# Kernel tuning notes

Hardware: AMD Instinct MI355X
Metric: run time of the kernel (lower is better)

## Reference

```python
import jax, jax.numpy as jnp
import numpy as np
import math

LS = [0, 1, 2]            # degrees present in all irreps
MAX_L = 2
MULT_IN = 64
MULT_MID = 16
MULT_OUT = 64
N = 20000

# ---- Clebsch-Gordan coefficients in the real spherical-harmonic basis ----

def _f(n):
    return math.factorial(int(n))

def _cg_complex(j1, m1, j2, m2, j3, m3):
    if m1 + m2 != m3:
        return 0.0
    pre = math.sqrt((2 * j3 + 1) * _f(j1 + j2 - j3) * _f(j1 - j2 + j3) * _f(-j1 + j2 + j3) / _f(j1 + j2 + j3 + 1))
    pre *= math.sqrt(_f(j1 + m1) * _f(j1 - m1) * _f(j2 + m2) * _f(j2 - m2) * _f(j3 + m3) * _f(j3 - m3))
    kmin = max(0, j2 - j3 - m1, j1 - j3 + m2)
    kmax = min(j1 + j2 - j3, j1 - m1, j2 + m2)
    s = 0.0
    for k in range(kmin, kmax + 1):
        s += (-1) ** k / (_f(k) * _f(j1 + j2 - j3 - k) * _f(j1 - m1 - k) * _f(j2 + m2 - k) * _f(j3 - j2 + m1 + k) * _f(j3 - j1 - m2 + k))
    return pre * s

def _q(l):
    # complex->real change of basis, rows indexed by real m = -l..l
    Q = np.zeros((2 * l + 1, 2 * l + 1), dtype=complex)
    Q[l, l] = 1.0
    r2 = math.sqrt(2.0)
    for m in range(1, l + 1):
        Q[l + m, l + m] = (-1) ** m / r2
        Q[l + m, l - m] = 1.0 / r2
        Q[l - m, l - m] = 1j / r2
        Q[l - m, l + m] = -1j * (-1) ** m / r2
    return Q

def _real_cg(l1, l2, l3):
    C = np.zeros((2 * l1 + 1, 2 * l2 + 1, 2 * l3 + 1), dtype=complex)
    for m1 in range(-l1, l1 + 1):
        for m2 in range(-l2, l2 + 1):
            m3 = m1 + m2
            if -l3 <= m3 <= l3:
                C[l1 + m1, l2 + m2, l3 + m3] = _cg_complex(l1, m1, l2, m2, l3, m3)
    Q1, Q2, Q3 = _q(l1), _q(l2), _q(l3)
    M = np.einsum('ia,jb,kc,abc->ijk', Q1.conj(), Q2.conj(), Q3, C)
    if np.abs(M.imag).max() > np.abs(M.real).max():
        M = M * (-1j)  # fix parity phase so coefficients are real
    assert np.abs(M.imag).max() < 1e-10
    return np.asarray(M.real, dtype=np.float32)

# triangle-rule paths, truncated at MAX_L
PATHS = [(l1, l2, l) for l1 in LS for l2 in LS for l in range(abs(l1 - l2), min(l1 + l2, MAX_L) + 1)]
CG = {p: jnp.asarray(_real_cg(*p)) for p in PATHS}


def setup_inputs() -> dict:
    key = jax.random.key(0)
    ks = jax.random.split(key, 12)
    inp = {}
    for i, l in enumerate(LS):
        inp[f'x{l}'] = jax.random.normal(ks[i], (N, MULT_IN, 2 * l + 1), dtype=jnp.float32)
    for i, l in enumerate(LS):
        inp[f'W1_{l}'] = jax.random.normal(ks[3 + i], (MULT_IN, MULT_MID), dtype=jnp.float32)
        inp[f'W2_{l}'] = jax.random.normal(ks[6 + i], (MULT_IN, MULT_MID), dtype=jnp.float32)
    tp_mults = {l: sum(MULT_MID * MULT_MID for (l1, l2, lo) in PATHS if lo == l) for l in LS}
    for i, l in enumerate(LS):
        inp[f'W3_{l}'] = jax.random.normal(ks[9 + i], (tp_mults[l], MULT_OUT), dtype=jnp.float32)
    return inp


def _linear(x, W):
    # x: [n, u, i], W: [u, v] -> [n, v, i], normalized like e3nn Linear
    return jnp.einsum('nui,uv->nvi', x, W) / np.float32(math.sqrt(x.shape[1]))


def reference(x0, x1, x2, W1_0, W1_1, W1_2, W2_0, W2_1, W2_2, W3_0, W3_1, W3_2):
    xs = [x0, x1, x2]
    W1 = [W1_0, W1_1, W1_2]
    W2 = [W2_0, W2_1, W2_2]
    W3 = [W3_0, W3_1, W3_2]
    a = [_linear(xs[l], W1[l]) for l in LS]   # branch 1
    b = [_linear(xs[l], W2[l]) for l in LS]   # branch 2
    # CG tensor product up to MAX_L, full (uv) multiplicity
    tp = {l: [] for l in LS}
    n = x0.shape[0]
    for (l1, l2, l) in PATHS:
        t = jnp.einsum('nui,nvj,ijk->nuvk', a[l1], b[l2], CG[(l1, l2, l)])
        tp[l].append(t.reshape(n, MULT_MID * MULT_MID, 2 * l + 1))
    outs = []
    for l in LS:
        z = jnp.concatenate(tp[l], axis=1)        # [n, tp_mult_l, 2l+1]
        y = _linear(z, W3[l])                     # [n, MULT_OUT, 2l+1]
        outs.append(y.reshape(n, -1))
    return jnp.concatenate(outs, axis=1)          # [n, MULT_OUT * 9]
```

## Files before the change

### kernel.cpp

```cpp
#include <hip/hip_runtime.h>


typedef __attribute__((ext_vector_type(4))) float f32x4;
typedef __attribute__((ext_vector_type(8))) short short8;
typedef unsigned short ushort_t;
typedef unsigned int uint32;

__device__ __forceinline__ uint32 bfb(float x) {
  uint32 u = __float_as_uint(x);
  return (u + 0x7fffu + ((u >> 16) & 1u)) >> 16;
}
__device__ __forceinline__ uint32 pack2(float lo, float hi) {
  return bfb(lo) | (bfb(hi) << 16);
}

#define C2   0.7071067811865476f
#define C3   0.5773502691896258f
#define C5   0.4472135954999579f
#define C6   0.4082482904638631f
#define C23  0.8164965809277260f
#define C10  0.3162277660168379f
#define C210 0.6324555320336759f
#define C310 0.5477225575051661f
#define C14  0.2672612419124244f
#define C214 0.5345224838248488f
#define C314 0.4629100498862757f

__global__ __launch_bounds__(256) void pack_w3_kernel(
    const float* __restrict__ W30, const float* __restrict__ W31,
    const float* __restrict__ W32, ushort_t* __restrict__ pack) {
  int lc = blockIdx.x;
  int t = threadIdx.x >> 6;
  int lam = threadIdx.x & 63;
  const float* W;
  int mb;
  float nrm;
  if (lc < 24) {
    W = W30; mb = lc * 32; nrm = 0.036084391824351615f;
  } else if (lc < 72) {
    W = W31; mb = (lc - 24) * 32; nrm = 0.025515518153991442f;
  } else {
    W = W32; mb = (lc - 72) * 32; nrm = 0.025515518153991442f;
  }
  int w = t * 16 + (lam & 15);
  int m0 = mb + (lam >> 4) * 8;
  ushort_t* dst = pack + ((size_t)(lc * 4 + t) * 64 + lam) * 8;
#pragma unroll
  for (int j = 0; j < 8; ++j)
    dst[j] = (ushort_t)bfb(W[(size_t)(m0 + j) * 64 + w] * nrm);
}

template <int NK, class F>
__device__ __forceinline__ void zgen_path(const float* bsrow, int boff, int s, int u,
                                          ushort_t* zs, F f) {
  uint32 zp[NK][8];
#pragma unroll
  for (int v2 = 0; v2 < 8; ++v2) {
    float z0[NK], z1[NK];
    f(bsrow + (2 * v2) * 12 + boff, z0);
    f(bsrow + (2 * v2 + 1) * 12 + boff, z1);
#pragma unroll
    for (int k = 0; k < NK; ++k) zp[k][v2] = pack2(z0[k], z1[k]);
  }
#pragma unroll
  for (int k = 0; k < NK; ++k) {
    uint32* dst = (uint32*)(zs + (k * 16 + s) * 264 + u * 16);
    *(uint4*)(dst) = make_uint4(zp[k][0], zp[k][1], zp[k][2], zp[k][3]);
    *(uint4*)(dst + 4) = make_uint4(zp[k][4], zp[k][5], zp[k][6], zp[k][7]);
  }
}

template <int NROW>
__device__ __forceinline__ void mfma_acc(const ushort_t* zs, const ushort_t* pack,
                                         int pcbase, int wt, int lane, f32x4* acc) {
  int srow = lane & 15, quad = lane >> 4;
  const ushort_t* ab = zs + srow * 264 + quad * 8;
  const ushort_t* bb = pack + ((size_t)(pcbase * 4 + wt) * 64 + lane) * 8;
#pragma unroll
  for (int c = 0; c < 8; ++c) {
    short8 B = *(const short8*)(bb + (size_t)c * 2048);
#pragma unroll
    for (int rt = 0; rt < NROW; ++rt) {
      short8 A = *(const short8*)(ab + rt * 16 * 264 + c * 32);
      acc[rt] = __builtin_amdgcn_mfma_f32_16x16x32_bf16(A, B, acc[rt], 0, 0, 0);
    }
  }
}

__global__ __launch_bounds__(256) void tdense_kernel(
    const float* __restrict__ x0, const float* __restrict__ x1,
    const float* __restrict__ x2, const float* __restrict__ W10,
    const float* __restrict__ W20, const float* __restrict__ W11,
    const float* __restrict__ W21, const float* __restrict__ W12,
    const float* __restrict__ W22, const ushort_t* __restrict__ pack,
    float* __restrict__ out) {
  __shared__ float a_s[2304];
  __shared__ float b_s[3072];
  __shared__ __align__(16) ushort_t z_s[21120];

  const int tid = threadIdx.x;
  const int nbase = blockIdx.x * 16;

  for (int it = tid; it < 512; it += 256) {
    int brn = it >> 8;
    int s = (it >> 4) & 15;
    int v = it & 15;
    int n = nbase + s;
    const float* Wl0 = brn ? W20 : W10;
    const float* Wl1 = brn ? W21 : W11;
    const float* Wl2 = brn ? W22 : W12;
    const float* px0 = x0 + (size_t)n * 64;
    const float* px1 = x1 + (size_t)n * 192;
    const float* px2 = x2 + (size_t)n * 320;
    float s0 = 0.f, s1a = 0.f, s1b = 0.f, s1c = 0.f;
    float s2[5] = {0.f, 0.f, 0.f, 0.f, 0.f};
    for (int u = 0; u < 64; ++u) {
      float w0 = Wl0[u * 16 + v];
      float w1 = Wl1[u * 16 + v];
      float w2 = Wl2[u * 16 + v];
      s0 += px0[u] * w0;
      s1a += px1[u * 3 + 0] * w1;
      s1b += px1[u * 3 + 1] * w1;
      s1c += px1[u * 3 + 2] * w1;
#pragma unroll
      for (int j = 0; j < 5; ++j) s2[j] += px2[u * 5 + j] * w2;
    }
    float* dst = brn ? (b_s + (s * 16 + v) * 12) : (a_s + (s * 16 + v) * 9);
    dst[0] = s0 * 0.125f;
    dst[1] = s1a * 0.125f;
    dst[2] = s1b * 0.125f;
    dst[3] = s1c * 0.125f;
#pragma unroll
    for (int j = 0; j < 5; ++j) dst[4 + j] = s2[j] * 0.125f;
  }

  const int lane = tid & 63, wt = tid >> 6;
  const int zs_s = tid >> 4, zu = tid & 15;

  f32x4 acc0[1], acc1[3], acc2[5];
#pragma unroll
  for (int i = 0; i < 1; ++i) acc0[i] = (f32x4)(0.f);
#pragma unroll
  for (int i = 0; i < 3; ++i) acc1[i] = (f32x4)(0.f);
#pragma unroll
  for (int i = 0; i < 5; ++i) acc2[i] = (f32x4)(0.f);

  __syncthreads();

  float ar[9];
  {
    const float* arow = a_s + (zs_s * 16 + zu) * 9;
#pragma unroll
    for (int i = 0; i < 9; ++i) ar[i] = arow[i];
  }
  const float* bsrow = b_s + zs_s * 16 * 12;

#define RUN_PATH(NK, BOFF, PC, ACC, BODY)                         \
  zgen_path<NK>(bsrow, BOFF, zs_s, zu, z_s,                       \
                [&](const float* b, float* z) BODY);              \
  __syncthreads();                                                \
  mfma_acc<NK>(z_s, pack, PC, wt, lane, ACC);                     \
  __syncthreads();

  RUN_PATH(1, 0, 0, acc0, { z[0] = ar[0] * b[0]; })
  RUN_PATH(3, 1, 24, acc1, {
    z[0] = ar[0] * b[0]; z[1] = ar[0] * b[1]; z[2] = ar[0] * b[2];
  })
  RUN_PATH(5, 4, 72, acc2, {
    z[0] = ar[0] * b[0]; z[1] = ar[0] * b[1]; z[2] = ar[0] * b[2];
    z[3] = ar[0] * b[3]; z[4] = ar[0] * b[4];
  })
  RUN_PATH(3, 0, 32, acc1, {
    z[0] = ar[1] * b[0]; z[1] = ar[2] * b[0]; z[2] = ar[3] * b[0];
  })
  RUN_PATH(1, 1, 8, acc0, {
    z[0] = -C3 * (ar[1] * b[0] + ar[2] * b[1] + ar[3] * b[2]);
  })
  RUN_PATH(3, 1, 40, acc1, {
    z[0] = C2 * (ar[2] * b[2] - ar[3] * b[1]);
    z[1] = C2 * (ar[3] * b[0] - ar[1] * b[2]);
    z[2] = C2 * (ar[1] * b[1] - ar[2] * b[0]);
  })
  RUN_PATH(5, 1, 80, acc2, {
    z[0] = C2 * (ar[1] * b[2] + ar[3] * b[0]);
    z[1] = C2 * (ar[2] * b[0] + ar[1] * b[1]);
    z[2] = C23 * ar[2] * b[1] - C6 * (ar[1] * b[0] + ar[3] * b[2]);
    z[3] = C2 * (ar[2] * b[2] + ar[3] * b[1]);
    z[4] = C2 * (ar[3] * b[2] - ar[1] * b[0]);
  })
  RUN_PATH(3, 4, 48, acc1, {
    z[0] = -C310 * ar[2] * b[1] + C10 * ar[1] * b[2] - C310 * ar[3] * b[0] + C310 * ar[1] * b[4];
    z[1] = -C210 * ar[2] * b[2] - C310 * ar[3] * b[3] - C310 * ar[1] * b[1];
    z[2] = -C310 * ar[2] * b[3] + C10 * ar[3] * b[2] - C310 * ar[1] * b[0] - C310 * ar[3] * b[4];
  })
  RUN_PATH(5, 4, 88, acc2, {
    z[0] = C23 * ar[2] * b[4] + C6 * ar[1] * b[1] - C6 * ar[3] * b[3];
    z[1] = C6 * ar[2] * b[3] - C6 * ar[1] * b[0] - C2 * ar[3] * b[2] - C6 * ar[3] * b[4];
    z[2] = C2 * (ar[3] * b[1] - ar[1] * b[3]);
    z[3] = -C6 * ar[2] * b[1] + C2 * ar[1] * b[2] + C6 * ar[3] * b[0] - C6 * ar[1] * b[4];
    z[4] = -C23 * ar[2] * b[0] + C6 * ar[1] * b[3] + C6 * ar[3] * b[1];
  })
  RUN_PATH(5, 0, 96, acc2, {
    z[0] = ar[4] * b[0]; z[1] = ar[5] * b[0]; z[2] = ar[6] * b[0];
    z[3] = ar[7] * b[0]; z[4] = ar[8] * b[0];
  })
  RUN_PATH(3, 1, 56, acc1, {
    z[0] = -C310 * ar[5] * b[1] + C10 * ar[6] * b[0] - C310 * ar[4] * b[2] + C310 * ar[8] * b[0];
    z[1] = -C210 * ar[6] * b[1] - C310 * ar[7] * b[2] - C310 * ar[5] * b[0];
    z[2] = -C310 * ar[7] * b[1] + C10 * ar[6] * b[2] - C310 * ar[4] * b[0] - C310 * ar[8] * b[2];
  })
  RUN_PATH(5, 1, 104, acc2, {
    z[0] = -C23 * ar[8] * b[1] - C6 * ar[5] * b[0] + C6 * ar[7] * b[2];
    z[1] = -C6 * ar[7] * b[1] + C6 * ar[4] * b[0] + C2 * ar[6] * b[2] + C6 * ar[8] * b[2];
    z[2] = C2 * (ar[7] * b[0] - ar[5] * b[2]);
    z[3] = C6 * ar[5] * b[1] - C2 * ar[6] * b[0] - C6 * ar[4] * b[2] + C6 * ar[8] * b[0];
    z[4] = C23 * ar[4] * b[1] - C6 * ar[7] * b[0] - C6 * ar[5] * b[2];
  })
  RUN_PATH(1, 4, 16, acc0, {
    z[0] = C5 * (ar[4] * b[0] + ar[5] * b[1] + ar[6] * b[2] + ar[7] * b[3] + ar[8] * b[4]);
  })
  RUN_PATH(3, 4, 64, acc1, {
    z[0] = C10 * (ar[8] * b[3] - ar[7] * b[4] + ar[4] * b[1] - ar[5] * b[0]) +
           C310 * (ar[7] * b[2] - ar[6] * b[3]);
    z[1] = C10 * (ar[5] * b[3] - ar[7] * b[1]) + C210 * (ar[4] * b[4] - ar[8] * b[0]);
    z[2] = C10 * (ar[8] * b[1] - ar[5] * b[4] + ar[7] * b[0] - ar[4] * b[3]) +
           C310 * (ar[6] * b[1] - ar[5] * b[2]);
  })
  RUN_PATH(5, 4, 112, acc2, {
    z[0] = C214 * (ar[6] * b[0] + ar[4] * b[2]) - C314 * (ar[5] * b[3] + ar[7] * b[1]);
    z[1] = -C14 * (ar[6] * b[1] + ar[5] * b[2]) + C314 * (ar[5] * b[4] + ar[8] * b[1]) -
           C314 * (ar[7] * b[0] + ar[4] * b[3]);
    z[2] = -C214 * ar[6] * b[2] - C14 * (ar[5] * b[1] + ar[7] * b[3]) +
           C214 * (ar[4] * b[0] + ar[8] * b[4]);
    z[3] = -C14 * (ar[6] * b[3] + ar[7] * b[2]) - C314 * (ar[5] * b[0] + ar[4] * b[1]) -
           C314 * (ar[7] * b[4] + ar[8] * b[3]);
    z[4] = C214 * (ar[6] * b[4] + ar[8] * b[2]) + C314 * (ar[5] * b[1] - ar[7] * b[3]);
  })
#undef RUN_PATH

  {
    const int col = lane & 15, quad = lane >> 4;
    const int w = wt * 16 + col;
#pragma unroll
    for (int r = 0; r < 4; ++r) {
      int s = quad * 4 + r;
      float* row = out + (size_t)(nbase + s) * 576;
      row[w] = acc0[0][r];
      row[64 + w * 3 + 0] = acc1[0][r];
      row[64 + w * 3 + 1] = acc1[1][r];
      row[64 + w * 3 + 2] = acc1[2][r];
#pragma unroll
      for (int k = 0; k < 5; ++k) row[256 + w * 5 + k] = acc2[k][r];
    }
  }
}

extern "C" void kernel_launch(void* const* d_in, const int* in_sizes, int n_in,
                              void* d_out, int out_size, void* d_ws, size_t ws_size,
                              hipStream_t stream) {
  const float* x0 = (const float*)d_in[0];
  const float* x1 = (const float*)d_in[1];
  const float* x2 = (const float*)d_in[2];
  const float* W10 = (const float*)d_in[3];
  const float* W20 = (const float*)d_in[4];
  const float* W11 = (const float*)d_in[5];
  const float* W21 = (const float*)d_in[6];
  const float* W12 = (const float*)d_in[7];
  const float* W22 = (const float*)d_in[8];
  const float* W30 = (const float*)d_in[9];
  const float* W31 = (const float*)d_in[10];
  const float* W32 = (const float*)d_in[11];
  ushort_t* pack = (ushort_t*)d_ws;

  hipLaunchKernelGGL(pack_w3_kernel, dim3(120), dim3(256), 0, stream,
                     W30, W31, W32, pack);

  int nsamp = in_sizes[0] / 64;
  int nblocks = nsamp / 16;
  hipLaunchKernelGGL(tdense_kernel, dim3(nblocks), dim3(256), 0, stream,
                     x0, x1, x2, W10, W20, W11, W21, W12, W22, pack,
                     (float*)d_out);
}
```

Before: 259.5 us.

## Batch CG paths per barrier, vectorize projections, cheaper bf16 packing

The first-stage projections now run in one pass per thread, computing both branches with vectorized float4 loads of x. The a-projection stays in registers, and b is stored transposed to shared memory so the z-generation can load it as vectors. Several CG paths are grouped into one shared-memory z buffer per synchronization phase, which cuts the number of barriers. The bf16 conversion switches to a cheaper round-half-up pack using a byte permute, which slightly changes the rounding behavior. The z buffer grows and launch_bounds now requests 2 blocks per CU, which may constrain registers.

Result: faster. 222.7 us (-14.2%).

```diff
diff --git a/kernel.cpp b/kernel.cpp
--- a/kernel.cpp
+++ b/kernel.cpp
@@ -2,6 +2,8 @@
 
 
 typedef __attribute__((ext_vector_type(4))) float f32x4;
+typedef __attribute__((ext_vector_type(4))) float f4;
+typedef __attribute__((ext_vector_type(2))) float f2;
 typedef __attribute__((ext_vector_type(8))) short short8;
 typedef unsigned short ushort_t;
 typedef unsigned int uint32;
@@ -10,8 +12,11 @@
   uint32 u = __float_as_uint(x);
   return (u + 0x7fffu + ((u >> 16) & 1u)) >> 16;
 }
-__device__ __forceinline__ uint32 pack2(float lo, float hi) {
-  return bfb(lo) | (bfb(hi) << 16);
+
+__device__ __forceinline__ uint32 pack2f(f2 z) {
+  uint32 lo = __float_as_uint(z.x) + 0x8000u;
+  uint32 hi = __float_as_uint(z.y) + 0x8000u;
+  return __builtin_amdgcn_perm(hi, lo, 0x07060302u);
 }
 
 #define C2   0.7071067811865476f
@@ -50,96 +55,131 @@
     dst[j] = (ushort_t)bfb(W[(size_t)(m0 + j) * 64 + w] * nrm);
 }
 
-template <int NK, class F>
-__device__ __forceinline__ void zgen_path(const float* bsrow, int boff, int s, int u,
-                                          ushort_t* zs, F f) {
+template <int NK, int JD, class F>
+__device__ __forceinline__ void zgenv(const float* bsj, ushort_t* zrow, F f) {
   uint32 zp[NK][8];
 #pragma unroll
-  for (int v2 = 0; v2 < 8; ++v2) {
-    float z0[NK], z1[NK];
-    f(bsrow + (2 * v2) * 12 + boff, z0);
-    f(bsrow + (2 * v2 + 1) * 12 + boff, z1);
-#pragma unroll
-    for (int k = 0; k < NK; ++k) zp[k][v2] = pack2(z0[k], z1[k]);
+  for (int oc = 0; oc < 2; ++oc) {
+    f2 bb4[JD][4];
+#pragma unroll
+    for (int j = 0; j < JD; ++j) {
+      f4 lo = *(const f4*)(bsj + j * 16 + oc * 8);
+      f4 hi = *(const f4*)(bsj + j * 16 + oc * 8 + 4);
+      bb4[j][0] = lo.xy; bb4[j][1] = lo.zw;
+      bb4[j][2] = hi.xy; bb4[j][3] = hi.zw;
+    }
+#pragma unroll
+    for (int q = 0; q < 4; ++q) {
+      f2 bcol[JD], z[NK];
+#pragma unroll
+      for (int j = 0; j < JD; ++j) bcol[j] = bb4[j][q];
+      f(bcol, z);
+#pragma unroll
+      for (int k = 0; k < NK; ++k) zp[k][oc * 4 + q] = pack2f(z[k]);
+    }
   }
 #pragma unroll
   for (int k = 0; k < NK; ++k) {
-    uint32* dst = (uint32*)(zs + (k * 16 + s) * 264 + u * 16);
-    *(uint4*)(dst) = make_uint4(zp[k][0], zp[k][1], zp[k][2], zp[k][3]);
-    *(uint4*)(dst + 4) = make_uint4(zp[k][4], zp[k][5], zp[k][6], zp[k][7]);
+    uint32* d = (uint32*)(zrow + k * (16 * 264));
+    *(uint4*)(d) = make_uint4(zp[k][0], zp[k][1], zp[k][2], zp[k][3]);
+    *(uint4*)(d + 4) = make_uint4(zp[k][4], zp[k][5], zp[k][6], zp[k][7]);
   }
 }
 
 template <int NROW>
 __device__ __forceinline__ void mfma_acc(const ushort_t* zs, const ushort_t* pack,
-                                         int pcbase, int wt, int lane, f32x4* acc) {
+                                         int kbase, int pcbase, int wt, int lane,
+                                         f32x4* acc) {
   int srow = lane & 15, quad = lane >> 4;
-  const ushort_t* ab = zs + srow * 264 + quad * 8;
+  const ushort_t* ab = zs + (kbase * 16 + srow) * 264 + quad * 8;
   const ushort_t* bb = pack + ((size_t)(pcbase * 4 + wt) * 64 + lane) * 8;
 #pragma unroll
   for (int c = 0; c < 8; ++c) {
     short8 B = *(const short8*)(bb + (size_t)c * 2048);
 #pragma unroll
     for (int rt = 0; rt < NROW; ++rt) {
-      short8 A = *(const short8*)(ab + rt * 16 * 264 + c * 32);
+      short8 A = *(const short8*)(ab + rt * (16 * 264) + c * 32);
       acc[rt] = __builtin_amdgcn_mfma_f32_16x16x32_bf16(A, B, acc[rt], 0, 0, 0);
     }
   }
 }
 
-__global__ __launch_bounds__(256) void tdense_kernel(
+__global__ __launch_bounds__(256, 2) void tdense_kernel(
     const float* __restrict__ x0, const float* __restrict__ x1,
     const float* __restrict__ x2, const float* __restrict__ W10,
     const float* __restrict__ W20, const float* __restrict__ W11,
     const float* __restrict__ W21, const float* __restrict__ W12,
     const float* __restrict__ W22, const ushort_t* __restrict__ pack,
     float* __restrict__ out) {
-  __shared__ float a_s[2304];
-  __shared__ float b_s[3072];
-  __shared__ __align__(16) ushort_t z_s[21120];
+  __shared__ float b_s[2368];
+  __shared__ __align__(16) ushort_t z_s[25344];
 
   const int tid = threadIdx.x;
   const int nbase = blockIdx.x * 16;
-
-  for (int it = tid; it < 512; it += 256) {
-    int brn = it >> 8;
-    int s = (it >> 4) & 15;
-    int v = it & 15;
-    int n = nbase + s;
-    const float* Wl0 = brn ? W20 : W10;
-    const float* Wl1 = brn ? W21 : W11;
-    const float* Wl2 = brn ? W22 : W12;
-    const float* px0 = x0 + (size_t)n * 64;
-    const float* px1 = x1 + (size_t)n * 192;
-    const float* px2 = x2 + (size_t)n * 320;
-    float s0 = 0.f, s1a = 0.f, s1b = 0.f, s1c = 0.f;
-    float s2[5] = {0.f, 0.f, 0.f, 0.f, 0.f};
-    for (int u = 0; u < 64; ++u) {
-      float w0 = Wl0[u * 16 + v];
-      float w1 = Wl1[u * 16 + v];
-      float w2 = Wl2[u * 16 + v];
-      s0 += px0[u] * w0;
-      s1a += px1[u * 3 + 0] * w1;
-      s1b += px1[u * 3 + 1] * w1;
-      s1c += px1[u * 3 + 2] * w1;
-#pragma unroll
-      for (int j = 0; j < 5; ++j) s2[j] += px2[u * 5 + j] * w2;
-    }
-    float* dst = brn ? (b_s + (s * 16 + v) * 12) : (a_s + (s * 16 + v) * 9);
-    dst[0] = s0 * 0.125f;
-    dst[1] = s1a * 0.125f;
-    dst[2] = s1b * 0.125f;
-    dst[3] = s1c * 0.125f;
-#pragma unroll
-    for (int j = 0; j < 5; ++j) dst[4 + j] = s2[j] * 0.125f;
+  const int s = tid >> 4, v = tid & 15;
+
+  const int n = nbase + s;
+  const float* px0 = x0 + (size_t)n * 64;
+  const float* px1 = x1 + (size_t)n * 192;
+  const float* px2 = x2 + (size_t)n * 320;
+  float a0 = 0.f, a1x = 0.f, a1y = 0.f, a1z = 0.f;
+  float a2[5] = {0.f, 0.f, 0.f, 0.f, 0.f};
+  float b0 = 0.f, b1x = 0.f, b1y = 0.f, b1z = 0.f;
+  float b2[5] = {0.f, 0.f, 0.f, 0.f, 0.f};
+  for (int u4 = 0; u4 < 16; ++u4) {
+    f4 xv0 = *(const f4*)(px0 + u4 * 4);
+    f4 xa = *(const f4*)(px1 + u4 * 12);
+    f4 xb = *(const f4*)(px1 + u4 * 12 + 4);
+    f4 xc = *(const f4*)(px1 + u4 * 12 + 8);
+    f4 ya = *(const f4*)(px2 + u4 * 20);
+    f4 yb = *(const f4*)(px2 + u4 * 20 + 4);
+    f4 yc = *(const f4*)(px2 + u4 * 20 + 8);
+    f4 yd = *(const f4*)(px2 + u4 * 20 + 12);
+    f4 ye = *(const f4*)(px2 + u4 * 20 + 16);
+    float x1e[12], x2e[20];
+#pragma unroll
+    for (int e = 0; e < 4; ++e) { x1e[e] = xa[e]; x1e[4 + e] = xb[e]; x1e[8 + e] = xc[e]; }
+#pragma unroll
+    for (int e = 0; e < 4; ++e) {
+      x2e[e] = ya[e]; x2e[4 + e] = yb[e]; x2e[8 + e] = yc[e];
+      x2e[12 + e] = yd[e]; x2e[16 + e] = ye[e];
+    }
+#pragma unroll
+    for (int r = 0; r < 4; ++r) {
+      int u = u4 * 4 + r;
+      float wa0 = W10[u * 16 + v], wb0 = W20[u * 16 + v];
+      float wa1 = W11[u * 16 + v], wb1 = W21[u * 16 + v];
+      float wa2 = W12[u * 16 + v], wb2 = W22[u * 16 + v];
+      float xx = xv0[r];
+      a0 += xx * wa0; b0 += xx * wb0;
+      float e0 = x1e[r * 3 + 0], e1 = x1e[r * 3 + 1], e2 = x1e[r * 3 + 2];
+      a1x += e0 * wa1; a1y += e1 * wa1; a1z += e2 * wa1;
+      b1x += e0 * wb1; b1y += e1 * wb1; b1z += e2 * wb1;
+#pragma unroll
+      for (int j = 0; j < 5; ++j) {
+        float ev = x2e[r * 5 + j];
+        a2[j] += ev * wa2;
+        b2[j] += ev * wb2;
+      }
+    }
+  }
+  const float inv8 = 0.125f;
+  float ar[9];
+  ar[0] = a0 * inv8;
+  ar[1] = a1x * inv8; ar[2] = a1y * inv8; ar[3] = a1z * inv8;
+#pragma unroll
+  for (int j = 0; j < 5; ++j) ar[4 + j] = a2[j] * inv8;
+  {
+    float* bw = b_s + s * 148 + v;
+    bw[0] = b0 * inv8;
+    bw[16] = b1x * inv8; bw[32] = b1y * inv8; bw[48] = b1z * inv8;
+#pragma unroll
+    for (int j = 0; j < 5; ++j) bw[64 + j * 16] = b2[j] * inv8;
   }
 
   const int lane = tid & 63, wt = tid >> 6;
-  const int zs_s = tid >> 4, zu = tid & 15;
-
   f32x4 acc0[1], acc1[3], acc2[5];
-#pragma unroll
-  for (int i = 0; i < 1; ++i) acc0[i] = (f32x4)(0.f);
+  acc0[0] = (f32x4)(0.f);
 #pragma unroll
   for (int i = 0; i < 3; ++i) acc1[i] = (f32x4)(0.f);
 #pragma unroll
@@ -147,86 +187,118 @@
 
   __syncthreads();
 
-  float ar[9];
-  {
-    const float* arow = a_s + (zs_s * 16 + zu) * 9;
-#pragma unroll
-    for (int i = 0; i < 9; ++i) ar[i] = arow[i];
-  }
-  const float* bsrow = b_s + zs_s * 16 * 12;
-
-#define RUN_PATH(NK, BOFF, PC, ACC, BODY)                         \
-  zgen_path<NK>(bsrow, BOFF, zs_s, zu, z_s,                       \
-                [&](const float* b, float* z) BODY);              \
-  __syncthreads();                                                \
-  mfma_acc<NK>(z_s, pack, PC, wt, lane, ACC);                     \
-  __syncthreads();
-
-  RUN_PATH(1, 0, 0, acc0, { z[0] = ar[0] * b[0]; })
-  RUN_PATH(3, 1, 24, acc1, {
+  const float* bsl0 = b_s + s * 148;
+  const float* bsl1 = b_s + s * 148 + 16;
+  const float* bsl2 = b_s + s * 148 + 64;
+  ushort_t* zr0 = z_s + s * 264 + v * 16;
+#define ZROW(kb) (zr0 + (kb) * (16 * 264))
+
+  zgenv<1, 1>(bsl0, ZROW(0), [&](const f2* b, f2* z) { z[0] = ar[0] * b[0]; });
+  zgenv<1, 3>(bsl1, ZROW(1), [&](const f2* b, f2* z) {
+    z[0] = -C3 * (ar[1] * b[0] + ar[2] * b[1] + ar[3] * b[2]);
+  });
+  zgenv<1, 5>(bsl2, ZROW(2), [&](const f2* b, f2* z) {
+    z[0] = C5 * (ar[4] * b[0] + ar[5] * b[1] + ar[6] * b[2] + ar[7] * b[3] + ar[8] * b[4]);
+  });
+  zgenv<3, 3>(bsl1, ZROW(3), [&](const f2* b, f2* z) {
     z[0] = ar[0] * b[0]; z[1] = ar[0] * b[1]; z[2] = ar[0] * b[2];
-  })
-  RUN_PATH(5, 4, 72, acc2, {
-    z[0] = ar[0] * b[0]; z[1] = ar[0] * b[1]; z[2] = ar[0] * b[2];
-    z[3] = ar[0] * b[3]; z[4] = ar[0] * b[4];
-  })
-  RUN_PATH(3, 0, 32, acc1, {
+  });
+  __syncthreads();
+  mfma_acc<1>(z_s, pack, 0, 0, wt, lane, acc0);
+  mfma_acc<1>(z_s, pack, 1, 8, wt, lane, acc0);
+  mfma_acc<1>(z_s, pack, 2, 16, wt, lane, acc0);
+  mfma_acc<3>(z_s, pack, 3, 24, wt, lane, acc1);
+  __syncthreads();
+
+  zgenv<3, 1>(bsl0, ZROW(0), [&](const f2* b, f2* z) {
     z[0] = ar[1] * b[0]; z[1] = ar[2] * b[0]; z[2] = ar[3] * b[0];
-  })
-  RUN_PATH(1, 1, 8, acc0, {
-    z[0] = -C3 * (ar[1] * b[0] + ar[2] * b[1] + ar[3] * b[2]);
-  })
-  RUN_PATH(3, 1, 40, acc1, {
+  });
+  zgenv<3, 3>(bsl1, ZROW(3), [&](const f2* b, f2* z) {
     z[0] = C2 * (ar[2] * b[2] - ar[3] * b[1]);
     z[1] = C2 * (ar[3] * b[0] - ar[1] * b[2]);
     z[2] = C2 * (ar[1] * b[1] - ar[2] * b[0]);
-  })
-  RUN_PATH(5, 1, 80, acc2, {
+  });
+  __syncthreads();
+  mfma_acc<3>(z_s, pack, 0, 32, wt, lane, acc1);
+  mfma_acc<3>(z_s, pack, 3, 40, wt, lane, acc1);
+  __syncthreads();
+
+  zgenv<3, 5>(bsl2, ZROW(0), [&](const f2* b, f2* z) {
+    z[0] = -C310 * ar[2] * b[1] + C10 * ar[1] * b[2] - C310 * ar[3] * b[0] + C310 * ar[1] * b[4];
+    z[1] = -C210 * ar[2] * b[2] - C310 * ar[3] * b[3] - C310 * ar[1] * b[1];
+    z[2] = -C310 * ar[2] * b[3] + C10 * ar[3] * b[2] - C310 * ar[1] * b[0] - C310 * ar[3] * b[4];
+  });
+  zgenv<3, 3>(bsl1, ZROW(3), [&](const f2* b, f2* z) {
+    z[0] = -C310 * ar[5] * b[1] + C10 * ar[6] * b[0] - C310 * ar[4] * b[2] + C310 * ar[8] * b[0];
+    z[1] = -C210 * ar[6] * b[1] - C310 * ar[7] * b[2] - C310 * ar[5] * b[0];
+    z[2] = -C310 * ar[7] * b[1] + C10 * ar[6] * b[2] - C310 * ar[4] * b[0] - C310 * ar[8] * b[2];
+  });
+  __syncthreads();
+  mfma_acc<3>(z_s, pack, 0, 48, wt, lane, acc1);
+  mfma_acc<3>(z_s, pack, 3, 56, wt, lane, acc1);
+  __syncthreads();
+
+  zgenv<3, 5>(bsl2, ZROW(0), [&](const f2* b, f2* z) {
+    z[0] = C10 * (ar[8] * b[3] - ar[7] * b[4] + ar[4] * b[1] - ar[5] * b[0]) +
+           C310 * (ar[7] * b[2] - ar[6] * b[3]);
+    z[1] = C10 * (ar[5] * b[3] - ar[7] * b[1]) + C210 * (ar[4] * b[4] - ar[8] * b[0]);
+    z[2] = C10 * (ar[8] * b[1] - ar[5] * b[4] + ar[7] * b[0] - ar[4] * b[3]) +
+           C310 * (ar[6] * b[1] - ar[5] * b[2]);
+  });
+  __syncthreads();
+  mfma_acc<3>(z_s, pack, 0, 64, wt, lane, acc1);
+  __syncthreads();
+
+  zgenv<5, 5>(bsl2, ZROW(0), [&](const f2* b, f2* z) {
+    z[0] = ar[0] * b[0]; z[1] = ar[0] * b[1]; z[2] = ar[0] * b[2];
+    z[3] = ar[0] * b[3]; z[4] = ar[0] * b[4];
+  });
+  __syncthreads();
+  mfma_acc<5>(z_s, pack, 0, 72, wt, lane, acc2);
+  __syncthreads();
+
+  zgenv<5, 3>(bsl1, ZROW(0), [&](const f2* b, f2* z) {
     z[0] = C2 * (ar[1] * b[2] + ar[3] * b[0]);
     z[1] = C2 * (ar[2] * b[0] + ar[1] * b[1]);
     z[2] = C23 * ar[2] * b[1] - C6 * (ar[1] * b[0] + ar[3] * b[2]);
     z[3] = C2 * (ar[2] * b[2] + ar[3] * b[1]);
     z[4] = C2 * (ar[3] * b[2] - ar[1] * b[0]);
-  })
-  RUN_PATH(3, 4, 48, acc1, {
-    z[0] = -C310 * ar[2] * b[1] + C10 * ar[1] * b[2] - C310 * ar[3] * b[0] + C310 * ar[1] * b[4];
-    z[1] = -C210 * ar[2] * b[2] - C310 * ar[3] * b[3] - C310 * ar[1] * b[1];
-    z[2] = -C310 * ar[2] * b[3] + C10 * ar[3] * b[2] - C310 * ar[1] * b[0] - C310 * ar[3] * b[4];
-  })
-  RUN_PATH(5, 4, 88, acc2, {
+  });
+  __syncthreads();
+  mfma_acc<5>(z_s, pack, 0, 80, wt, lane, acc2);
+  __syncthreads();
+
+  zgenv<5, 5>(bsl2, ZROW(0), [&](const f2* b, f2* z) {
     z[0] = C23 * ar[2] * b[4] + C6 * ar[1] * b[1] - C6 * ar[3] * b[3];
     z[1] = C6 * ar[2] * b[3] - C6 * ar[1] * b[0] - C2 * ar[3] * b[2] - C6 * ar[3] * b[4];
     z[2] = C2 * (ar[3] * b[1] - ar[1] * b[3]);
     z[3] = -C6 * ar[2] * b[1] + C2 * ar[1] * b[2] + C6 * ar[3] * b[0] - C6 * ar[1] * b[4];
     z[4] = -C23 * ar[2] * b[0] + C6 * ar[1] * b[3] + C6 * ar[3] * b[1];
-  })
-  RUN_PATH(5, 0, 96, acc2, {
+  });
+  __syncthreads();
+  mfma_acc<5>(z_s, pack, 0, 88, wt, lane, acc2);
+  __syncthreads();
+
+  zgenv<5, 1>(bsl0, ZROW(0), [&](const f2* b, f2* z) {
     z[0] = ar[4] * b[0]; z[1] = ar[5] * b[0]; z[2] = ar[6] * b[0];
     z[3] = ar[7] * b[0]; z[4] = ar[8] * b[0];
-  })
-  RUN_PATH(3, 1, 56, acc1, {
-    z[0] = -C310 * ar[5] * b[1] + C10 * ar[6] * b[0] - C310 * ar[4] * b[2] + C310 * ar[8] * b[0];
-    z[1] = -C210 * ar[6] * b[1] - C310 * ar[7] * b[2] - C310 * ar[5] * b[0];
-    z[2] = -C310 * ar[7] * b[1] + C10 * ar[6] * b[2] - C310 * ar[4] * b[0] - C310 * ar[8] * b[2];
-  })
-  RUN_PATH(5, 1, 104, acc2, {
+  });
+  __syncthreads();
+  mfma_acc<5>(z_s, pack, 0, 96, wt, lane, acc2);
+  __syncthreads();
+
+  zgenv<5, 3>(bsl1, ZROW(0), [&](const f2* b, f2* z) {
     z[0] = -C23 * ar[8] * b[1] - C6 * ar[5] * b[0] + C6 * ar[7] * b[2];
     z[1] = -C6 * ar[7] * b[1] + C6 * ar[4] * b[0] + C2 * ar[6] * b[2] + C6 * ar[8] * b[2];
     z[2] = C2 * (ar[7] * b[0] - ar[5] * b[2]);
     z[3] = C6 * ar[5] * b[1] - C2 * ar[6] * b[0] - C6 * ar[4] * b[2] + C6 * ar[8] * b[0];
     z[4] = C23 * ar[4] * b[1] - C6 * ar[7] * b[0] - C6 * ar[5] * b[2];
-  })
-  RUN_PATH(1, 4, 16, acc0, {
-    z[0] = C5 * (ar[4] * b[0] + ar[5] * b[1] + ar[6] * b[2] + ar[7] * b[3] + ar[8] * b[4]);
-  })
-  RUN_PATH(3, 4, 64, acc1, {
-    z[0] = C10 * (ar[8] * b[3] - ar[7] * b[4] + ar[4] * b[1] - ar[5] * b[0]) +
-           C310 * (ar[7] * b[2] - ar[6] * b[3]);
-    z[1] = C10 * (ar[5] * b[3] - ar[7] * b[1]) + C210 * (ar[4] * b[4] - ar[8] * b[0]);
-    z[2] = C10 * (ar[8] * b[1] - ar[5] * b[4] + ar[7] * b[0] - ar[4] * b[3]) +
-           C310 * (ar[6] * b[1] - ar[5] * b[2]);
-  })
-  RUN_PATH(5, 4, 112, acc2, {
+  });
+  __syncthreads();
+  mfma_acc<5>(z_s, pack, 0, 104, wt, lane, acc2);
+  __syncthreads();
+
+  zgenv<5, 5>(bsl2, ZROW(0), [&](const f2* b, f2* z) {
     z[0] = C214 * (ar[6] * b[0] + ar[4] * b[2]) - C314 * (ar[5] * b[3] + ar[7] * b[1]);
     z[1] = -C14 * (ar[6] * b[1] + ar[5] * b[2]) + C314 * (ar[5] * b[4] + ar[8] * b[1]) -
            C314 * (ar[7] * b[0] + ar[4] * b[3]);
@@ -235,16 +307,18 @@
     z[3] = -C14 * (ar[6] * b[3] + ar[7] * b[2]) - C314 * (ar[5] * b[0] + ar[4] * b[1]) -
            C314 * (ar[7] * b[4] + ar[8] * b[3]);
     z[4] = C214 * (ar[6] * b[4] + ar[8] * b[2]) + C314 * (ar[5] * b[1] - ar[7] * b[3]);
-  })
-#undef RUN_PATH
+  });
+  __syncthreads();
+  mfma_acc<5>(z_s, pack, 0, 112, wt, lane, acc2);
+#undef ZROW
 
   {
     const int col = lane & 15, quad = lane >> 4;
     const int w = wt * 16 + col;
 #pragma unroll
     for (int r = 0; r < 4; ++r) {
-      int s = quad * 4 + r;
-      float* row = out + (size_t)(nbase + s) * 576;
+      int so = quad * 4 + r;
+      float* row = out + (size_t)(nbase + so) * 576;
       row[w] = acc0[0][r];
       row[64 + w * 3 + 0] = acc1[0][r];
       row[64 + w * 3 + 1] = acc1[1][r];
```
